# Performance work log

Hardware: AMD Instinct MI355X
Metric: run time of the kernel (lower is better)

Reference implementation:

```python
import jax, jax.numpy as jnp
import numpy as np
import math

B, H, S, DK = 2, 16, 2048, 64

def setup_inputs() -> dict:
    key = jax.random.key(0)
    kq, kk, kv, km = jax.random.split(key, 4)
    q = jax.random.normal(kq, (B, H, S, DK), dtype=jnp.float32)
    k = jax.random.normal(kk, (B, H, S, DK), dtype=jnp.float32)
    v = jax.random.normal(kv, (B, H, S, DK), dtype=jnp.float32)
    mask = jax.random.randint(km, (1, 1, S, S), 0, 2).astype(jnp.bool_)
    return {"q": q, "k": k, "v": v, "mask": mask}

def reference(q, k, v, mask):
    d_k = q.shape[-1]
    # scores: [B,H,Sq,Sk]
    scores = jnp.einsum('bhqd,bhkd->bhqk', q, k) / math.sqrt(d_k)
    scores = jnp.where(mask, jnp.float32(-1e9), scores)
    # NOTE: original uses nn.Softmax(dim=2) -> softmax over the QUERY axis
    attn = jax.nn.softmax(scores, axis=2)
    out = jnp.einsum('bhqk,bhkd->bhqd', attn, v)
    return out
```

## Files before the change

kernel.cpp:

```cpp
#include <hip/hip_runtime.h>
#include <math.h>

#define S_LEN 2048
#define NCH   32
#define N_BH  32

typedef short bf16x8 __attribute__((ext_vector_type(8)));
typedef _Float16 f16x8 __attribute__((ext_vector_type(8)));
typedef _Float16 f16x4 __attribute__((ext_vector_type(4)));
typedef float f32x4  __attribute__((ext_vector_type(4)));
typedef unsigned short u16;
typedef unsigned short u16x8 __attribute__((ext_vector_type(8)));
typedef unsigned long long u64;

#define MFMA32(a,b,c) __builtin_amdgcn_mfma_f32_16x16x32_bf16((a),(b),(c),0,0,0)
#define MFMAH(a,b,c)  __builtin_amdgcn_mfma_f32_16x16x32_f16((a),(b),(c),0,0,0)
#define EXP2(x) __builtin_amdgcn_exp2f(x)

__device__ __forceinline__ f32x4 mfma16(f16x4 a, f16x4 b, f32x4 c) {
#if __has_builtin(__builtin_amdgcn_mfma_f32_16x16x16f16)
  return __builtin_amdgcn_mfma_f32_16x16x16f16(a, b, c, 0, 0, 0);
#else
  const _Float16 z = (_Float16)0.0f;
  f16x8 a8 = {a[0], a[1], a[2], a[3], z, z, z, z};
  f16x8 b8 = {b[0], b[1], b[2], b[3], z, z, z, z};
  return MFMAH(a8, b8, c);
#endif
}

#define SC        0.18033688011112042f
#define MASKED_L2 (-14.0f)

__device__ __forceinline__ u16 f2h(float x) {
  union { _Float16 h; u16 u; } v;
  v.h = (_Float16)x;
  return v.u;
}
__device__ __forceinline__ u16 f2bf_rne(float x) {
  unsigned u = __float_as_uint(x);
  return (u16)((u + 0x7FFF + ((u >> 16) & 1)) >> 16);
}
__device__ __forceinline__ void bfsplit(float x, u16& h, u16& l) {
  unsigned u = __float_as_uint(x);
  h = (u16)(u >> 16);
  float hf = __uint_as_float(u & 0xFFFF0000u);
  l = f2bf_rne(x - hf);
}

__global__ __launch_bounds__(256) void pack_mask(
    const int* __restrict__ mask, u64* __restrict__ bits) {
  const int word = blockIdx.x * 4 + (threadIdx.x >> 6);
  const int lane = threadIdx.x & 63;
  const int row = word >> 5, wc = word & 31;
  int m = mask[(size_t)row * S_LEN + wc * 64 + lane];
  u64 b = __ballot(m != 0);
  if (lane == 0) bits[word] = b;
}

__global__ __launch_bounds__(256) void prep_qk(
    const float* __restrict__ Q, const float* __restrict__ K,
    u16* __restrict__ qf, u16* __restrict__ kf) {
  const int tid = threadIdx.x;
  const int slot = tid & 15, r0 = tid >> 4;
  const size_t rowbase = (size_t)blockIdx.x * 64;
#pragma unroll
  for (int p = 0; p < 4; ++p) {
    const size_t row = rowbase + p * 16 + r0;
    const size_t dst = row * 64 + ((slot * 4) ^ (((int)row & 7) << 3));
    float4 xq = *(const float4*)(Q + row * 64 + slot * 4);
    *(ushort4*)(qf + dst) = make_ushort4(
        f2h(xq.x * SC), f2h(xq.y * SC), f2h(xq.z * SC), f2h(xq.w * SC));
    float4 xk = *(const float4*)(K + row * 64 + slot * 4);
    *(ushort4*)(kf + dst) = make_ushort4(
        f2h(xk.x), f2h(xk.y), f2h(xk.z), f2h(xk.w));
  }
}

__global__ __launch_bounds__(256) void prep_w(
    const float* __restrict__ V, const float* __restrict__ part,
    u16* __restrict__ w_t) {
  __shared__ __align__(16) u16 ts[4096];
  const int tid = threadIdx.x;
  const int kc = blockIdx.x, bh = blockIdx.y;
  const int k = tid >> 2, dblk = (tid & 3) * 16;
  const size_t ko = (size_t)bh * S_LEN + kc * 64 + k;
  const float lsum = part[ko] + part[65536 + ko];
  const float ilk = 1.0f / lsum;
  const float* vb = V + ko * 64 + dblk;
#pragma unroll
  for (int u = 0; u < 4; ++u) {
    float4 x = *(const float4*)(vb + u * 4);
    float xs[4] = {x.x, x.y, x.z, x.w};
#pragma unroll
    for (int e = 0; e < 4; ++e) {
      const int d = dblk + u * 4 + e;
      ts[d * 64 + (k ^ ((d & 7) << 3))] = f2h(xs[e] * ilk);
    }
  }
  __syncthreads();
  u16* dst = w_t + ((size_t)bh * NCH + kc) * 4096;
#pragma unroll
  for (int j = 0; j < 2; ++j)
    *(u16x8*)(dst + j * 2048 + tid * 8) = *(const u16x8*)(ts + j * 2048 + tid * 8);
}

__global__ __launch_bounds__(512, 4) void passA(
    const u16* __restrict__ qf, const u16* __restrict__ kf,
    const u64* __restrict__ mbits, float* __restrict__ part) {
  __shared__ __align__(16) u16 qbuf[4096];

  const int tid = threadIdx.x;
  const int lane = tid & 63;
  const int w = tid >> 6;
  const int c = lane & 15;
  const int g = lane >> 4;
  const int bx = blockIdx.x;
  const int bh = blockIdx.y;
  const int qp = blockIdx.z;

  const size_t bh_off = (size_t)bh * S_LEN * 64;
  const int swc = (c & 7) << 3;

  f16x8 ka[2][2];
#pragma unroll
  for (int t = 0; t < 2; ++t) {
    const int row = bx * 256 + w * 32 + t * 16 + c;
#pragma unroll
    for (int h = 0; h < 2; ++h)
      ka[t][h] = *(const f16x8*)(kf + bh_off + (size_t)row * 64
                                 + ((h * 32 + g * 8) ^ swc));
  }

  u16x8 stg = *(const u16x8*)(qf + bh_off + (size_t)(qp * 1024) * 64 + tid * 8);

  float lp[2][4] = {{0.f, 0.f, 0.f, 0.f}, {0.f, 0.f, 0.f, 0.f}};
  const int word = bx * 4 + (w >> 1);
  const int sh0 = (w & 1) * 32;

  for (int qs = 0; qs < 16; ++qs) {
    __syncthreads();
    *(u16x8*)(qbuf + tid * 8) = stg;
    __syncthreads();
    if (qs + 1 < 16)
      stg = *(const u16x8*)(qf + bh_off
            + (size_t)(qp * 1024 + (qs + 1) * 64) * 64 + tid * 8);

#pragma unroll
    for (int sub = 0; sub < 4; ++sub) {
      f16x8 fh[2];
      const int rb = sub * 1024 + c * 64;
#pragma unroll
      for (int h = 0; h < 2; ++h)
        fh[h] = *(const f16x8*)(qbuf + rb + ((h * 32 + g * 8) ^ swc));
      const int qrow = qp * 1024 + qs * 64 + sub * 16 + c;
      const u64 mw = mbits[(size_t)qrow * NCH + word];
#pragma unroll
      for (int t = 0; t < 2; ++t) {
        f32x4 acc = {0.f, 0.f, 0.f, 0.f};
        acc = MFMAH(ka[t][0], fh[0], acc);
        acc = MFMAH(ka[t][1], fh[1], acc);
        const unsigned nib = (unsigned)(mw >> (sh0 + t * 16 + g * 4)) & 0xFu;
#pragma unroll
        for (int r = 0; r < 4; ++r) {
          const float s = ((nib >> r) & 1) ? MASKED_L2 : acc[r];
          lp[t][r] += EXP2(s);
        }
      }
    }
  }

#pragma unroll
  for (int off = 1; off < 16; off <<= 1)
#pragma unroll
    for (int t = 0; t < 2; ++t)
#pragma unroll
      for (int r = 0; r < 4; ++r) lp[t][r] += __shfl_xor(lp[t][r], off, 64);
  if (c == 0) {
#pragma unroll
    for (int t = 0; t < 2; ++t) {
      float4 o = {lp[t][0], lp[t][1], lp[t][2], lp[t][3]};
      *(float4*)(part + (size_t)qp * 65536 + (size_t)bh * S_LEN
                 + bx * 256 + w * 32 + t * 16 + g * 4) = o;
    }
  }
}

__global__ __launch_bounds__(256, 4) void passC(
    const u16* __restrict__ qf, const u16* __restrict__ kf,
    const u16* __restrict__ w_t, const u64* __restrict__ mbits,
    float* __restrict__ out) {
  __shared__ __align__(16) u16 sbuf[8192];

  const int tid = threadIdx.x;
  const int lane = tid & 63;
  const int w = tid >> 6;
  const int c = lane & 15;
  const int g = lane >> 4;
  const int qc = blockIdx.x;
  const int bh = blockIdx.y;

  const size_t bh_off = (size_t)bh * S_LEN * 64;
  const u16* tb_k = kf + bh_off;
  const u16* tb_w = w_t + (size_t)bh * NCH * 4096;
  const int swc = (c & 7) << 3;

  int qrow[2];
  f16x8 qb[2][2];
#pragma unroll
  for (int u = 0; u < 2; ++u) {
    qrow[u] = qc * 128 + w * 32 + u * 16 + c;
#pragma unroll
    for (int h = 0; h < 2; ++h)
      qb[u][h] = *(const f16x8*)(qf + bh_off + (size_t)qrow[u] * 64
                                 + ((h * 32 + g * 8) ^ swc));
  }

  f32x4 oacc[2][4];
#pragma unroll
  for (int u = 0; u < 2; ++u)
#pragma unroll
    for (int dt = 0; dt < 4; ++dt) oacc[u][dt] = (f32x4){0.f, 0.f, 0.f, 0.f};

  const int so = tid * 8;

  u16x8 stg[4];
#pragma unroll
  for (int j = 0; j < 2; ++j) {
    stg[0 + j] = *(const u16x8*)(tb_k + j * 2048 + so);
    stg[2 + j] = *(const u16x8*)(tb_w + j * 2048 + so);
  }

  for (int kc = 0; kc < NCH; ++kc) {
    __syncthreads();
#pragma unroll
    for (int j = 0; j < 2; ++j) {
      *(u16x8*)(sbuf + j * 2048 + so) = stg[0 + j];
      *(u16x8*)(sbuf + 4096 + j * 2048 + so) = stg[2 + j];
    }
    __syncthreads();
    if (kc + 1 < NCH) {
      const size_t nb = (size_t)(kc + 1) * 4096;
#pragma unroll
      for (int j = 0; j < 2; ++j) {
        stg[0 + j] = *(const u16x8*)(tb_k + nb + j * 2048 + so);
        stg[2 + j] = *(const u16x8*)(tb_w + nb + j * 2048 + so);
      }
    }

    const u64 mw0 = mbits[(size_t)qrow[0] * NCH + kc];
    const u64 mw1 = mbits[(size_t)qrow[1] * NCH + kc];

#pragma unroll
    for (int kt = 0; kt < 4; ++kt) {
      const int kbase = (16 * kt + c) * 64;
      f16x8 ak0 = *(const f16x8*)(sbuf + kbase + ((g * 8) ^ swc));
      f16x8 ak1 = *(const f16x8*)(sbuf + kbase + ((32 + g * 8) ^ swc));
      f16x4 pf0, pf1;
#pragma unroll
      for (int u = 0; u < 2; ++u) {
        f32x4 acc = {0.f, 0.f, 0.f, 0.f};
        acc = MFMAH(ak0, qb[u][0], acc);
        acc = MFMAH(ak1, qb[u][1], acc);
        const u64 mwu = u ? mw1 : mw0;
        const unsigned nib = (unsigned)(mwu >> (kt * 16 + g * 4)) & 0xFu;
        f16x4 pf;
#pragma unroll
        for (int r = 0; r < 4; ++r) {
          const float s = ((nib >> r) & 1) ? MASKED_L2 : acc[r];
          pf[r] = (_Float16)EXP2(s);
        }
        if (u == 0) pf0 = pf; else pf1 = pf;
      }
#pragma unroll
      for (int dt = 0; dt < 4; ++dt) {
        const int aoff = 4096 + (16 * dt + c) * 64 + ((16 * kt + 4 * g) ^ swc);
        f16x4 av = *(const f16x4*)(sbuf + aoff);
        oacc[0][dt] = mfma16(av, pf0, oacc[0][dt]);
        oacc[1][dt] = mfma16(av, pf1, oacc[1][dt]);
      }
    }
  }

#pragma unroll
  for (int u = 0; u < 2; ++u) {
    float* ob = out + (bh_off + (size_t)qrow[u] * 64);
#pragma unroll
    for (int dt = 0; dt < 4; ++dt) {
      float4 o = {oacc[u][dt][0], oacc[u][dt][1], oacc[u][dt][2], oacc[u][dt][3]};
      *(float4*)(ob + dt * 16 + g * 4) = o;
    }
  }
}

__global__ __launch_bounds__(256) void passA_colsum(
    const float* __restrict__ Q, const float* __restrict__ K,
    const u64* __restrict__ mbits, float* __restrict__ il_out) {
  const int tid = threadIdx.x;
  const int lane = tid & 63;
  const int w = tid >> 6;
  const int c = lane & 15;
  const int g = lane >> 4;
  const int kc = blockIdx.x;
  const int bh = blockIdx.y;

  const float* Qb = Q + (size_t)bh * S_LEN * 64;
  const float* Kb = K + (size_t)bh * S_LEN * 64;

  bf16x8 kah[2], kal[2];
  {
    const int krow = kc * 64 + w * 16 + c;
#pragma unroll
    for (int h = 0; h < 2; ++h) {
      const float* src = Kb + (size_t)krow * 64 + h * 32 + g * 8;
      float4 x = *(const float4*)(src);
      float4 y = *(const float4*)(src + 4);
      float xs[8] = {x.x, x.y, x.z, x.w, y.x, y.y, y.z, y.w};
#pragma unroll
      for (int e = 0; e < 8; ++e) {
        u16 hh, ll; bfsplit(xs[e], hh, ll);
        kah[h][e] = (short)hh; kal[h][e] = (short)ll;
      }
    }
  }

  float lp[4] = {0.f, 0.f, 0.f, 0.f};
  const int shift = w * 16 + g * 4;

  for (int qs = 0; qs < S_LEN / 16; ++qs) {
    const int qrow = qs * 16 + c;
    bf16x8 qbh_[2], qbl_[2];
#pragma unroll
    for (int h = 0; h < 2; ++h) {
      const float* src = Qb + (size_t)qrow * 64 + h * 32 + g * 8;
      float4 x = *(const float4*)(src);
      float4 y = *(const float4*)(src + 4);
      float xs[8] = {x.x, x.y, x.z, x.w, y.x, y.y, y.z, y.w};
#pragma unroll
      for (int e = 0; e < 8; ++e) {
        u16 hh, ll; bfsplit(xs[e] * SC, hh, ll);
        qbh_[h][e] = (short)hh; qbl_[h][e] = (short)ll;
      }
    }
    f32x4 acc = {0.f, 0.f, 0.f, 0.f};
#pragma unroll
    for (int h = 0; h < 2; ++h) {
      acc = MFMA32(kah[h], qbh_[h], acc);
      acc = MFMA32(kal[h], qbh_[h], acc);
      acc = MFMA32(kah[h], qbl_[h], acc);
    }
    u64 mw = mbits[(size_t)qrow * NCH + kc];
    unsigned nib = (unsigned)(mw >> shift) & 0xFu;
#pragma unroll
    for (int r = 0; r < 4; ++r) {
      float s = ((nib >> r) & 1) ? -30.0f : acc[r];
      lp[r] += exp2f(s);
    }
  }
#pragma unroll
  for (int off = 1; off < 16; off <<= 1)
#pragma unroll
    for (int r = 0; r < 4; ++r) lp[r] += __shfl_xor(lp[r], off, 64);
  if (c == 0) {
    float4 o = {1.f / lp[0], 1.f / lp[1], 1.f / lp[2], 1.f / lp[3]};
    *(float4*)(il_out + (size_t)bh * S_LEN + kc * 64 + w * 16 + g * 4) = o;
  }
}

__global__ __launch_bounds__(256) void passC_out(
    const float* __restrict__ Q, const float* __restrict__ K,
    const float* __restrict__ V, const u64* __restrict__ mbits,
    const float* __restrict__ il_in, float* __restrict__ out) {
  __shared__ u16 kh_s[4096];
  __shared__ u16 kl_s[4096];
  __shared__ u16 vt_s[4096];
  __shared__ u16 p_s[4096];

  const int tid = threadIdx.x;
  const int lane = tid & 63;
  const int w = tid >> 6;
  const int c = lane & 15;
  const int g = lane >> 4;
  const int qc = blockIdx.x;
  const int bh = blockIdx.y;

  const float* Qb = Q + (size_t)bh * S_LEN * 64;
  const float* Kb = K + (size_t)bh * S_LEN * 64;
  const float* Vb = V + (size_t)bh * S_LEN * 64;

  bf16x8 qbh_[2], qbl_[2];
  {
    const int qrow = qc * 64 + w * 16 + c;
#pragma unroll
    for (int h = 0; h < 2; ++h) {
      const float* src = Qb + (size_t)qrow * 64 + h * 32 + g * 8;
      float4 x = *(const float4*)(src);
      float4 y = *(const float4*)(src + 4);
      float xs[8] = {x.x, x.y, x.z, x.w, y.x, y.y, y.z, y.w};
#pragma unroll
      for (int e = 0; e < 8; ++e) {
        u16 hh, ll; bfsplit(xs[e] * SC, hh, ll);
        qbh_[h][e] = (short)hh; qbl_[h][e] = (short)ll;
      }
    }
  }

  f32x4 oacc[4];
#pragma unroll
  for (int dt = 0; dt < 4; ++dt) oacc[dt] = (f32x4){0.f, 0.f, 0.f, 0.f};

  const int slot = tid & 15, r0 = tid >> 4;
  const int kv = tid & 63, dblk = tid >> 6;
  const int swc = (c & 7) << 3;
  const int pbase = w * 1024 + c * 64;

  for (int kc = 0; kc < NCH; ++kc) {
    __syncthreads();
#pragma unroll
    for (int p = 0; p < 4; ++p) {
      const int row = p * 16 + r0;
      float4 kx = *(const float4*)(Kb + (size_t)(kc * 64 + row) * 64 + slot * 4);
      float xs[4] = {kx.x, kx.y, kx.z, kx.w};
      u16 ha[4], la[4];
#pragma unroll
      for (int e = 0; e < 4; ++e) bfsplit(xs[e], ha[e], la[e]);
      const int idx = row * 64 + ((slot * 4) ^ ((row & 7) << 3));
      *(ushort4*)(kh_s + idx) = make_ushort4(ha[0], ha[1], ha[2], ha[3]);
      *(ushort4*)(kl_s + idx) = make_ushort4(la[0], la[1], la[2], la[3]);
    }
    {
      const float ilk = il_in[(size_t)bh * S_LEN + kc * 64 + kv];
#pragma unroll
      for (int u = 0; u < 4; ++u) {
        float4 vv = *(const float4*)(Vb + (size_t)(kc * 64 + kv) * 64 + dblk * 16 + u * 4);
        float xs[4] = {vv.x, vv.y, vv.z, vv.w};
#pragma unroll
        for (int e = 0; e < 4; ++e) {
          const int d = dblk * 16 + u * 4 + e;
          vt_s[d * 64 + (kv ^ ((d & 7) << 3))] = f2bf_rne(xs[e] * ilk);
        }
      }
    }
    __syncthreads();

    const u64 mw = mbits[(size_t)(qc * 64 + w * 16 + c) * NCH + kc];

#pragma unroll
    for (int kt = 0; kt < 4; ++kt) {
      const int kbase = (16 * kt + c) * 64;
      bf16x8 akh[2], akl[2];
#pragma unroll
      for (int h = 0; h < 2; ++h) {
        const int off = (h * 32 + g * 8) ^ swc;
        akh[h] = *(const bf16x8*)(kh_s + kbase + off);
        akl[h] = *(const bf16x8*)(kl_s + kbase + off);
      }
      f32x4 acc = {0.f, 0.f, 0.f, 0.f};
#pragma unroll
      for (int h = 0; h < 2; ++h) {
        acc = MFMA32(akh[h], qbh_[h], acc);
        acc = MFMA32(akl[h], qbh_[h], acc);
        acc = MFMA32(akh[h], qbl_[h], acc);
      }
      const unsigned nib = (unsigned)(mw >> (kt * 16 + g * 4)) & 0xFu;
      u16 pb[4];
#pragma unroll
      for (int r = 0; r < 4; ++r) {
        const float s = ((nib >> r) & 1) ? -30.0f : acc[r];
        pb[r] = f2bf_rne(exp2f(s));
      }
      *(ushort4*)(p_s + pbase + ((kt * 16 + g * 4) ^ swc)) =
          make_ushort4(pb[0], pb[1], pb[2], pb[3]);
    }
    __syncthreads();

#pragma unroll
    for (int s = 0; s < 2; ++s) {
      const int koff = (s * 32 + 8 * g) ^ swc;
      bf16x8 pb8 = *(const bf16x8*)(p_s + pbase + koff);
#pragma unroll
      for (int dt = 0; dt < 4; ++dt) {
        bf16x8 av = *(const bf16x8*)(vt_s + (16 * dt + c) * 64 + koff);
        oacc[dt] = MFMA32(av, pb8, oacc[dt]);
      }
    }
  }

  float* ob = out + ((size_t)bh * S_LEN + qc * 64 + w * 16 + c) * 64;
#pragma unroll
  for (int dt = 0; dt < 4; ++dt) {
    float4 o = {oacc[dt][0], oacc[dt][1], oacc[dt][2], oacc[dt][3]};
    *(float4*)(ob + dt * 16 + g * 4) = o;
  }
}

extern "C" void kernel_launch(void* const* d_in, const int* in_sizes, int n_in,
                              void* d_out, int out_size, void* d_ws, size_t ws_size,
                              hipStream_t stream) {
  (void)in_sizes; (void)n_in; (void)out_size;
  const float* q = (const float*)d_in[0];
  const float* k = (const float*)d_in[1];
  const float* v = (const float*)d_in[2];
  const int* mask = (const int*)d_in[3];
  float* out = (float*)d_out;

  u64* mbits = (u64*)d_ws;
  float* part = (float*)((char*)d_ws + 524288);
  const size_t PL = (size_t)N_BH * S_LEN * 64;
  u16* qf = (u16*)((char*)d_ws + 524288 + 1048576);
  u16* kf = qf + PL;
  u16* w_t = kf + PL;
  const size_t need = 524288 + 1048576 + 3 * PL * sizeof(u16);

  pack_mask<<<dim3(S_LEN * NCH / 4), 256, 0, stream>>>(mask, mbits);

  if (ws_size >= need) {
    prep_qk<<<dim3(1024), 256, 0, stream>>>(q, k, qf, kf);
    passA<<<dim3(8, N_BH, 2), 512, 0, stream>>>(qf, kf, mbits, part);
    prep_w<<<dim3(NCH, N_BH), 256, 0, stream>>>(v, part, w_t);
    passC<<<dim3(S_LEN / 128, N_BH), 256, 0, stream>>>(qf, kf, w_t, mbits, out);
  } else {
    float* il = part;
    dim3 grid(NCH, N_BH);
    passA_colsum<<<grid, 256, 0, stream>>>(q, k, mbits, il);
    passC_out<<<grid, 256, 0, stream>>>(q, k, v, mbits, il, out);
  }
}
```

Measured before the change: 131.8 us.

## Double-buffer passC LDS tiles and permute W layout for 128-bit reads

passC now keeps two LDS buffers and writes the next chunk into the alternate buffer after compute, so each iteration needs one barrier instead of two. prep_w permutes the k index within each row of the transposed W tile so that passC can read V/W operands as 8-wide f16 vectors and split them into two MFMA inputs, halving LDS read instructions. Probabilities are computed for all four k-subtiles before the PV MFMAs. LDS doubles to 32KB per block and launch bounds drop to 2 blocks per CU, which may reduce occupancy.

Measured after the change: 136.0 us. 3.2% more time.

```diff
diff --git a/kernel.cpp b/kernel.cpp
--- a/kernel.cpp
+++ b/kernel.cpp
@@ -83,6 +83,9 @@
   const int tid = threadIdx.x;
   const int kc = blockIdx.x, bh = blockIdx.y;
   const int k = tid >> 2, dblk = (tid & 3) * 16;
+  const int kt = k >> 4, gg = (k >> 2) & 3, r = k & 3;
+  const int sub = (kt & 1) * 4 + r;
+  const int lu = gg * 2 + (kt >> 1);
   const size_t ko = (size_t)bh * S_LEN + kc * 64 + k;
   const float lsum = part[ko] + part[65536 + ko];
   const float ilk = 1.0f / lsum;
@@ -94,7 +97,7 @@
 #pragma unroll
     for (int e = 0; e < 4; ++e) {
       const int d = dblk + u * 4 + e;
-      ts[d * 64 + (k ^ ((d & 7) << 3))] = f2h(xs[e] * ilk);
+      ts[d * 64 + (((lu ^ (d & 7)) << 3) + sub)] = f2h(xs[e] * ilk);
     }
   }
   __syncthreads();
@@ -185,11 +188,11 @@
   }
 }
 
-__global__ __launch_bounds__(256, 4) void passC(
+__global__ __launch_bounds__(256, 2) void passC(
     const u16* __restrict__ qf, const u16* __restrict__ kf,
     const u16* __restrict__ w_t, const u64* __restrict__ mbits,
     float* __restrict__ out) {
-  __shared__ __align__(16) u16 sbuf[8192];
+  __shared__ __align__(16) u16 sbuf[2][8192];
 
   const int tid = threadIdx.x;
   const int lane = tid & 63;
@@ -229,15 +232,15 @@
     stg[0 + j] = *(const u16x8*)(tb_k + j * 2048 + so);
     stg[2 + j] = *(const u16x8*)(tb_w + j * 2048 + so);
   }
-
+#pragma unroll
+  for (int j = 0; j < 2; ++j) {
+    *(u16x8*)(&sbuf[0][0] + j * 2048 + so) = stg[0 + j];
+    *(u16x8*)(&sbuf[0][0] + 4096 + j * 2048 + so) = stg[2 + j];
+  }
+  __syncthreads();
+
+  int cur = 0;
   for (int kc = 0; kc < NCH; ++kc) {
-    __syncthreads();
-#pragma unroll
-    for (int j = 0; j < 2; ++j) {
-      *(u16x8*)(sbuf + j * 2048 + so) = stg[0 + j];
-      *(u16x8*)(sbuf + 4096 + j * 2048 + so) = stg[2 + j];
-    }
-    __syncthreads();
     if (kc + 1 < NCH) {
       const size_t nb = (size_t)(kc + 1) * 4096;
 #pragma unroll
@@ -247,15 +250,16 @@
       }
     }
 
+    const u16* bufc = &sbuf[cur][0];
     const u64 mw0 = mbits[(size_t)qrow[0] * NCH + kc];
     const u64 mw1 = mbits[(size_t)qrow[1] * NCH + kc];
 
+    f16x4 pf[2][4];
 #pragma unroll
     for (int kt = 0; kt < 4; ++kt) {
       const int kbase = (16 * kt + c) * 64;
-      f16x8 ak0 = *(const f16x8*)(sbuf + kbase + ((g * 8) ^ swc));
-      f16x8 ak1 = *(const f16x8*)(sbuf + kbase + ((32 + g * 8) ^ swc));
-      f16x4 pf0, pf1;
+      f16x8 ak0 = *(const f16x8*)(bufc + kbase + ((g * 8) ^ swc));
+      f16x8 ak1 = *(const f16x8*)(bufc + kbase + ((32 + g * 8) ^ swc));
 #pragma unroll
       for (int u = 0; u < 2; ++u) {
         f32x4 acc = {0.f, 0.f, 0.f, 0.f};
@@ -263,22 +267,40 @@
         acc = MFMAH(ak1, qb[u][1], acc);
         const u64 mwu = u ? mw1 : mw0;
         const unsigned nib = (unsigned)(mwu >> (kt * 16 + g * 4)) & 0xFu;
-        f16x4 pf;
 #pragma unroll
         for (int r = 0; r < 4; ++r) {
           const float s = ((nib >> r) & 1) ? MASKED_L2 : acc[r];
-          pf[r] = (_Float16)EXP2(s);
+          pf[u][kt][r] = (_Float16)EXP2(s);
         }
-        if (u == 0) pf0 = pf; else pf1 = pf;
-      }
+      }
+    }
+
+#pragma unroll
+    for (int ktp = 0; ktp < 2; ++ktp) {
 #pragma unroll
       for (int dt = 0; dt < 4; ++dt) {
-        const int aoff = 4096 + (16 * dt + c) * 64 + ((16 * kt + 4 * g) ^ swc);
-        f16x4 av = *(const f16x4*)(sbuf + aoff);
-        oacc[0][dt] = mfma16(av, pf0, oacc[0][dt]);
-        oacc[1][dt] = mfma16(av, pf1, oacc[1][dt]);
-      }
-    }
+        const int aoff = 4096 + (16 * dt + c) * 64
+                       + (((g * 2 + ktp) ^ (c & 7)) << 3);
+        f16x8 av = *(const f16x8*)(bufc + aoff);
+        f16x4 alo = {av[0], av[1], av[2], av[3]};
+        f16x4 ahi = {av[4], av[5], av[6], av[7]};
+        oacc[0][dt] = mfma16(alo, pf[0][ktp * 2], oacc[0][dt]);
+        oacc[0][dt] = mfma16(ahi, pf[0][ktp * 2 + 1], oacc[0][dt]);
+        oacc[1][dt] = mfma16(alo, pf[1][ktp * 2], oacc[1][dt]);
+        oacc[1][dt] = mfma16(ahi, pf[1][ktp * 2 + 1], oacc[1][dt]);
+      }
+    }
+
+    if (kc + 1 < NCH) {
+      u16* bufn = &sbuf[cur ^ 1][0];
+#pragma unroll
+      for (int j = 0; j < 2; ++j) {
+        *(u16x8*)(bufn + j * 2048 + so) = stg[0 + j];
+        *(u16x8*)(bufn + 4096 + j * 2048 + so) = stg[2 + j];
+      }
+    }
+    __syncthreads();
+    cur ^= 1;
   }
 
 #pragma unroll
```
